# Performance work log

Hardware: AMD Instinct MI355X
Metric: run time of the kernel (lower is better)

The kernel has to match this reference:

```python
import jax, jax.numpy as jnp
import numpy as np


def setup_inputs() -> dict:
    key = jax.random.key(0)
    ks = jax.random.split(key, 6)
    N, C, T, V = 32, 64, 128, 25
    F = C * T * V  # 204800
    H = 256
    E = 4
    stdv0 = 1.0 / np.sqrt(F)
    stdv1 = 1.0 / np.sqrt(H)
    stdvA = 1.0 / np.sqrt(V)
    return {
        "x": jax.random.normal(ks[0], (N, C, T, V), dtype=jnp.float32),
        "W0": jax.random.uniform(ks[1], (F, H), jnp.float32, -stdv0, stdv0),
        "b0": jnp.zeros((H,), jnp.float32),
        "W1": jax.random.uniform(ks[2], (H, H), jnp.float32, -stdv1, stdv1),
        "b1": jnp.zeros((H,), jnp.float32),
        "W2": jax.random.uniform(ks[3], (H, E), jnp.float32, -stdv1, stdv1),
        "b2": jnp.zeros((E,), jnp.float32),
        "A": jax.random.uniform(ks[4], (E, T, V, V), jnp.float32, -stdvA, stdvA),
    }


def reference(x, W0, b0, W1, b1, W2, b2, A):
    N = x.shape[0]
    # Gating MLP (dropout treated as identity / eval mode)
    g = x.reshape(N, -1)                      # [N, C*T*V]
    h = jax.nn.elu(g @ W0 + b0)               # [N, 256]
    h = jax.nn.elu(h @ W1 + b1)               # [N, 256]
    logits = h @ W2 + b2                      # [N, 4]
    w = jax.nn.softmax(logits, axis=1)        # [N, 4]
    # Mixture of adjacency experts: AS[n,t,v,w] = sum_e w[n,e] * A[e,t,v,w]
    AS = jnp.einsum('ne,etvw->ntvw', w, A)    # [N, T, V, V]
    # Batched graph convolution
    out = jnp.einsum('nctv,ntvw->nctw', x, AS)
    return out
```

## Files before the change

### kernel.cpp

```cpp
#include <hip/hip_runtime.h>
#include <math.h>

#define Nn 32
#define Cc 64
#define Tt 128
#define Vv 25
#define Kk 204800
#define Hh 256
#define Ee 4
#define KC 128
#define NBLK_A 1600

__device__ __forceinline__ float elu1(float v) { return v > 0.0f ? v : expm1f(v); }

typedef const __attribute__((address_space(1))) void* gvp;
typedef __attribute__((address_space(3))) void* lvp;
__device__ __forceinline__ void gl_lds16(const void* g, void* l) {
  __builtin_amdgcn_global_load_lds((gvp)g, (lvp)l, 16, 0, 0);
}

typedef float v4f __attribute__((ext_vector_type(4)));

__global__ __launch_bounds__(256) void kA(const float* __restrict__ x,
                                          const float* __restrict__ W0,
                                          float* __restrict__ partials) {
  __shared__ float xs[Nn][KC];
  const int tid  = threadIdx.x;
  const int lane = tid & 63;
  const int wv   = tid >> 6;
  const int b  = blockIdx.x;
  const int k0 = b * KC;

  for (int rp = wv; rp < 16; rp += 4) {
    const int row = 2 * rp + (lane >> 5);
    gl_lds16(x + (size_t)row * Kk + k0 + (lane & 31) * 4, &xs[2 * rp][0]);
  }

  const int h0 = lane * 4;
  const int n0 = wv * 8;
  const float* W0p = W0 + (size_t)k0 * Hh + h0;

  float acc[8][4];
  #pragma unroll
  for (int i = 0; i < 8; ++i)
    #pragma unroll
    for (int c = 0; c < 4; ++c) acc[i][c] = 0.0f;

  __syncthreads();

  #pragma unroll 2
  for (int kk = 0; kk < KC; kk += 4) {
    v4f wr[4];
    #pragma unroll
    for (int u = 0; u < 4; ++u)
      wr[u] = *(const v4f*)(W0p + (size_t)(kk + u) * Hh);
    v4f xv[8];
    #pragma unroll
    for (int i = 0; i < 8; ++i)
      xv[i] = *(const v4f*)&xs[n0 + i][kk];
    #pragma unroll
    for (int u = 0; u < 4; ++u)
      #pragma unroll
      for (int i = 0; i < 8; ++i) {
        float xu = xv[i][u];
        acc[i][0] = fmaf(xu, wr[u][0], acc[i][0]);
        acc[i][1] = fmaf(xu, wr[u][1], acc[i][1]);
        acc[i][2] = fmaf(xu, wr[u][2], acc[i][2]);
        acc[i][3] = fmaf(xu, wr[u][3], acc[i][3]);
      }
  }

  #pragma unroll
  for (int i = 0; i < 8; ++i)
    *(v4f*)&partials[((size_t)(b * Nn + n0 + i) << 8) + h0] =
        (v4f){acc[i][0], acc[i][1], acc[i][2], acc[i][3]};
}

__global__ __launch_bounds__(256) void kB1(const float* __restrict__ partials,
                                           const float* __restrict__ b0,
                                           float* __restrict__ hb) {
  const int n  = blockIdx.x >> 3;
  const int hc = blockIdx.x & 7;
  const int tid = threadIdx.x;
  const int hl = tid & 31;
  const int bsub = tid >> 5;
  const int h = hc * 32 + hl;
  float s = 0.0f;
  for (int j = 0; j < 200; ++j) {
    int b = bsub * 200 + j;
    s += partials[((size_t)(b * Nn + n) << 8) + h];
  }
  __shared__ float red[8][32];
  red[bsub][hl] = s;
  __syncthreads();
  if (tid < 32) {
    float tot = 0.0f;
    #pragma unroll
    for (int sI = 0; sI < 8; ++sI) tot += red[sI][tid];
    int hh = hc * 32 + tid;
    hb[n * Hh + hh] = elu1(tot + b0[hh]);
  }
}

__global__ __launch_bounds__(256) void kB2(const float* __restrict__ hb,
                                           const float* __restrict__ W1,
                                           const float* __restrict__ b1,
                                           const float* __restrict__ W2,
                                           const float* __restrict__ b2,
                                           float* __restrict__ wgt) {
  const int n = blockIdx.x;
  const int tid = threadIdx.x;
  __shared__ float hbs[Hh];
  hbs[tid] = hb[n * Hh + tid];
  __syncthreads();
  float s = b1[tid];
  for (int j = 0; j < Hh; ++j) s = fmaf(hbs[j], W1[j * Hh + tid], s);
  float h2 = elu1(s);
  float le[Ee];
  #pragma unroll
  for (int e = 0; e < Ee; ++e) le[e] = h2 * W2[tid * Ee + e];
  __shared__ float red[Ee][4];
  const int lane = tid & 63;
  const int wid  = tid >> 6;
  #pragma unroll
  for (int e = 0; e < Ee; ++e) {
    float v = le[e];
    for (int off = 32; off > 0; off >>= 1) v += __shfl_down(v, off, 64);
    if (lane == 0) red[e][wid] = v;
  }
  __syncthreads();
  if (tid == 0) {
    float lg[Ee];
    float m = -1e30f;
    #pragma unroll
    for (int e = 0; e < Ee; ++e) {
      lg[e] = red[e][0] + red[e][1] + red[e][2] + red[e][3] + b2[e];
      m = fmaxf(m, lg[e]);
    }
    float den = 0.0f;
    #pragma unroll
    for (int e = 0; e < Ee; ++e) { lg[e] = expf(lg[e] - m); den += lg[e]; }
    float inv = 1.0f / den;
    #pragma unroll
    for (int e = 0; e < Ee; ++e) wgt[n * Ee + e] = lg[e] * inv;
  }
}

#define ASW 28
#define XTS 68
__global__ __launch_bounds__(256) void kC(const float* __restrict__ x,
                                          const float* __restrict__ A,
                                          const float* __restrict__ wgt,
                                          float* __restrict__ out) {
  const int blk = blockIdx.x;
  const int n  = blk >> 6;
  const int tp = blk & 63;
  const int tid = threadIdx.x;
  const int tsub = tid >> 7;
  const int tl = tid & 127;
  const int t = tp * 2 + tsub;

  __shared__ float AS[2][Vv][ASW];
  __shared__ float xT[2][Vv][XTS];

  float wv[Ee];
  #pragma unroll
  for (int e = 0; e < Ee; ++e) wv[e] = wgt[n * Ee + e];

  for (int idx = tl; idx < Vv * ASW; idx += 128) {
    int v = idx / ASW;
    int w = idx - v * ASW;
    float s = 0.0f;
    if (w < Vv) {
      #pragma unroll
      for (int e = 0; e < Ee; ++e)
        s = fmaf(wv[e], A[((size_t)(e * Tt + t) * Vv + v) * Vv + w], s);
    }
    AS[tsub][v][w] = s;
  }
  const float* xb = x + (size_t)n * (Cc * Tt * Vv) + (size_t)t * Vv;
  for (int idx = tl; idx < Cc * Vv; idx += 128) {
    int c = idx / Vv;
    int v = idx - c * Vv;
    xT[tsub][v][c] = xb[(size_t)c * (Tt * Vv) + v];
  }
  __syncthreads();

  const int ct = tl & 15;
  const int wq = tl >> 4;
  if (wq < 7) {
    const int c0 = ct * 4;
    const int w0 = wq * 4;
    float acc[4][4];
    #pragma unroll
    for (int i = 0; i < 4; ++i)
      #pragma unroll
      for (int j = 0; j < 4; ++j) acc[i][j] = 0.0f;
    #pragma unroll 5
    for (int v = 0; v < Vv; ++v) {
      float4 a4 = *(const float4*)&AS[tsub][v][w0];
      float4 x4 = *(const float4*)&xT[tsub][v][c0];
      const float xr[4] = {x4.x, x4.y, x4.z, x4.w};
      const float ar[4] = {a4.x, a4.y, a4.z, a4.w};
      #pragma unroll
      for (int i = 0; i < 4; ++i)
        #pragma unroll
        for (int j = 0; j < 4; ++j)
          acc[i][j] = fmaf(xr[i], ar[j], acc[i][j]);
    }
    #pragma unroll
    for (int i = 0; i < 4; ++i) {
      int c = c0 + i;
      float* ob = out + ((size_t)(n * Cc + c) * Tt + t) * Vv;
      #pragma unroll
      for (int j = 0; j < 4; ++j) {
        int w = w0 + j;
        if (w < Vv) ob[w] = acc[i][j];
      }
    }
  }
}

extern "C" void kernel_launch(void* const* d_in, const int* in_sizes, int n_in,
                              void* d_out, int out_size, void* d_ws, size_t ws_size,
                              hipStream_t stream) {
  const float* x  = (const float*)d_in[0];
  const float* W0 = (const float*)d_in[1];
  const float* b0 = (const float*)d_in[2];
  const float* W1 = (const float*)d_in[3];
  const float* b1 = (const float*)d_in[4];
  const float* W2 = (const float*)d_in[5];
  const float* b2 = (const float*)d_in[6];
  const float* A  = (const float*)d_in[7];
  float* out = (float*)d_out;

  float* partials = (float*)d_ws;
  float* hb  = partials + (size_t)NBLK_A * Nn * Hh;
  float* wgt = hb + Nn * Hh;

  kA <<<NBLK_A,  256, 0, stream>>>(x, W0, partials);
  kB1<<<256,     256, 0, stream>>>(partials, b0, hb);
  kB2<<<Nn,      256, 0, stream>>>(hb, W1, b1, W2, b2, wgt);
  kC <<<Nn * 64, 256, 0, stream>>>(x, A, wgt, out);
}
```

Measured before the change: 409.0 us.

## Split kA K-chunk across wave pairs with LDS reduction and coalesced partial stores

Reworks the kA thread mapping so each wave covers all 32 batch rows for 128 hidden columns over half of the 128-wide K chunk. Each thread now loads 2 W0 columns per k instead of 4, so each W0 element is read by only one wave instead of all four. The two K halves are summed in a reused 32KB LDS buffer, which is then written out as coalesced float4 stores. The cost is 64 accumulator registers per thread, extra syncs, and a larger LDS footprint that may lower occupancy.

```diff
diff --git a/kernel.cpp b/kernel.cpp
--- a/kernel.cpp
+++ b/kernel.cpp
@@ -20,14 +20,20 @@
 }
 
 typedef float v4f __attribute__((ext_vector_type(4)));
+typedef float v2f __attribute__((ext_vector_type(2)));
 
 __global__ __launch_bounds__(256) void kA(const float* __restrict__ x,
                                           const float* __restrict__ W0,
                                           float* __restrict__ partials) {
-  __shared__ float xs[Nn][KC];
+  __shared__ float smem[Nn * Hh];
+  float (*xs)[KC] = (float(*)[KC])smem;
+  float (*red)[Hh] = (float(*)[Hh])smem;
+
   const int tid  = threadIdx.x;
   const int lane = tid & 63;
   const int wv   = tid >> 6;
+  const int slice = wv & 1;
+  const int half  = wv >> 1;
   const int b  = blockIdx.x;
   const int k0 = b * KC;
 
@@ -36,44 +42,53 @@
     gl_lds16(x + (size_t)row * Kk + k0 + (lane & 31) * 4, &xs[2 * rp][0]);
   }
 
-  const int h0 = lane * 4;
-  const int n0 = wv * 8;
-  const float* W0p = W0 + (size_t)k0 * Hh + h0;
-
-  float acc[8][4];
-  #pragma unroll
-  for (int i = 0; i < 8; ++i)
-    #pragma unroll
-    for (int c = 0; c < 4; ++c) acc[i][c] = 0.0f;
-
-  __syncthreads();
-
-  #pragma unroll 2
-  for (int kk = 0; kk < KC; kk += 4) {
-    v4f wr[4];
+  const int h0 = half * 128 + lane * 2;
+  const int ks = slice * 64;
+  const float* W0p = W0 + ((size_t)k0 + ks) * Hh + h0;
+
+  v2f acc[Nn];
+  #pragma unroll
+  for (int n = 0; n < Nn; ++n) acc[n] = (v2f){0.0f, 0.0f};
+
+  __syncthreads();
+
+  #pragma unroll 1
+  for (int kk = 0; kk < 64; kk += 4) {
+    v2f wr[4];
     #pragma unroll
     for (int u = 0; u < 4; ++u)
-      wr[u] = *(const v4f*)(W0p + (size_t)(kk + u) * Hh);
-    v4f xv[8];
-    #pragma unroll
-    for (int i = 0; i < 8; ++i)
-      xv[i] = *(const v4f*)&xs[n0 + i][kk];
-    #pragma unroll
-    for (int u = 0; u < 4; ++u)
-      #pragma unroll
-      for (int i = 0; i < 8; ++i) {
-        float xu = xv[i][u];
-        acc[i][0] = fmaf(xu, wr[u][0], acc[i][0]);
-        acc[i][1] = fmaf(xu, wr[u][1], acc[i][1]);
-        acc[i][2] = fmaf(xu, wr[u][2], acc[i][2]);
-        acc[i][3] = fmaf(xu, wr[u][3], acc[i][3]);
+      wr[u] = *(const v2f*)(W0p + (size_t)(kk + u) * Hh);
+    #pragma unroll
+    for (int n = 0; n < Nn; ++n) {
+      v4f xv = *(const v4f*)&xs[n][ks + kk];
+      #pragma unroll
+      for (int u = 0; u < 4; ++u) {
+        acc[n][0] = fmaf(xv[u], wr[u][0], acc[n][0]);
+        acc[n][1] = fmaf(xv[u], wr[u][1], acc[n][1]);
       }
-  }
-
-  #pragma unroll
-  for (int i = 0; i < 8; ++i)
-    *(v4f*)&partials[((size_t)(b * Nn + n0 + i) << 8) + h0] =
-        (v4f){acc[i][0], acc[i][1], acc[i][2], acc[i][3]};
+    }
+  }
+
+  __syncthreads();
+  if (slice == 0) {
+    #pragma unroll
+    for (int n = 0; n < Nn; ++n) *(v2f*)&red[n][h0] = acc[n];
+  }
+  __syncthreads();
+  if (slice == 1) {
+    #pragma unroll
+    for (int n = 0; n < Nn; ++n) {
+      v2f r = *(v2f*)&red[n][h0];
+      r[0] += acc[n][0]; r[1] += acc[n][1];
+      *(v2f*)&red[n][h0] = r;
+    }
+  }
+  __syncthreads();
+
+  float* pb = partials + (size_t)b * (Nn * Hh);
+  #pragma unroll
+  for (int j = tid; j < (Nn * Hh) / 4; j += 256)
+    *(float4*)&pb[j * 4] = *(const float4*)&smem[j * 4];
 }
 
 __global__ __launch_bounds__(256) void kB1(const float* __restrict__ partials,
```

New measurement: 389.5 us. 4.7% less time.
